# Kernel tuning notes

Hardware: AMD Instinct MI355X
Metric: run time of the kernel (lower is better)

## Reference

```python
import jax, jax.numpy as jnp
import numpy as np

B, SQ, SK, D = 8, 4096, 4096, 128


def setup_inputs() -> dict:
    key = jax.random.key(0)
    kq, kk, kv = jax.random.split(key, 3)
    return {
        "q1": jax.random.normal(kq, (B, SQ, D), dtype=jnp.float32),
        "k1": jax.random.normal(kk, (B, SK, D), dtype=jnp.float32),
        "v1": jax.random.normal(kv, (B, SK, D), dtype=jnp.float32),
        "inv_scale_factor": jnp.float32(np.sqrt(D)),  # QK is divided by this
        "dropout_p": jnp.float32(0.1),
        "dropout_m": jnp.float32(0.1),
        "dropout_inplace": 1,  # no-op in functional JAX
    }


def reference(q1, k1, v1, inv_scale_factor, dropout_p, dropout_m, dropout_inplace):
    # qk = q1 @ k1^T ; scaled = qk / inv_scale_factor ; softmax over keys
    qk = jnp.einsum("bqd,bkd->bqk", q1, k1)
    softmax_qk = jax.nn.softmax(qk / inv_scale_factor, axis=-1)
    # torch: mask = F.dropout(ones_like(sm), p) -> bernoulli(1-p)/(1-p)
    keep = jax.random.bernoulli(jax.random.key(42), 1.0 - dropout_p, softmax_qk.shape)
    mask = keep.astype(softmax_qk.dtype) / (1.0 - dropout_p)
    # non-standard: divide by (1 - dropout_m) instead of (1 - dropout_p)
    dropout_qk = softmax_qk * mask / (1.0 - dropout_m)
    return jnp.einsum("bqk,bkd->bqd", dropout_qk, v1)
```

## Files before the change

kernel.cpp:

```cpp
#include <hip/hip_runtime.h>
#include <stdint.h>

#define Bn  8
#define SQn 4096
#define SKn 4096
#define Dn  128
#define QTn 64
#define KTn 64

typedef __attribute__((ext_vector_type(8))) short short8;
typedef __attribute__((ext_vector_type(4))) short short4v;
typedef __attribute__((ext_vector_type(4))) float f32x4;

__device__ __forceinline__ short f2bf(float f) {
  uint32_t x = __float_as_uint(f);
  uint32_t r = (x + 0x7FFFu + ((x >> 16) & 1u)) >> 16;
  return (short)r;
}

__device__ __forceinline__ uint32_t rotl32(uint32_t x, int r) {
  return __builtin_amdgcn_alignbit(x, x, (32 - r) & 31);
}

__device__ __forceinline__ uint32_t tf2x32_xor(uint32_t x0, uint32_t x1) {
  const uint32_t k0 = 0u, k1 = 42u, k2 = 0x1BD11BF0u;
  x0 += k0; x1 += k1;
#define TFR(r) { x0 += x1; x1 = rotl32(x1, r); x1 ^= x0; }
  TFR(13) TFR(15) TFR(26) TFR(6)  x0 += k1; x1 += k2 + 1u;
  TFR(17) TFR(29) TFR(16) TFR(24) x0 += k2; x1 += k0 + 2u;
  TFR(13) TFR(15) TFR(26) TFR(6)  x0 += k0; x1 += k1 + 3u;
  TFR(17) TFR(29) TFR(16) TFR(24) x0 += k1; x1 += k2 + 4u;
  TFR(13) TFR(15) TFR(26) TFR(6)  x0 += k2; x1 += k0 + 5u;
#undef TFR
  return x0 ^ x1;
}

template <int N>
__device__ __forceinline__ float ror16(float x) {
  int xi = __float_as_int(x);
  int r = __builtin_amdgcn_update_dpp(xi, xi, 0x120 | N, 0xF, 0xF, false);
  return __int_as_float(r);
}
__device__ __forceinline__ float redmax16(float x) {
  x = fmaxf(x, ror16<8>(x)); x = fmaxf(x, ror16<4>(x));
  x = fmaxf(x, ror16<2>(x)); x = fmaxf(x, ror16<1>(x));
  return x;
}
__device__ __forceinline__ float redsum16(float x) {
  x += ror16<8>(x); x += ror16<4>(x); x += ror16<2>(x); x += ror16<1>(x);
  return x;
}

__global__ __launch_bounds__(256, 2) void attn(
    const float* __restrict__ Qg, const float* __restrict__ Kg, const float* __restrict__ Vg,
    const float* __restrict__ p_inv, const float* __restrict__ p_pd, const float* __restrict__ p_pm,
    float* __restrict__ Out) {
  __shared__ __align__(16) short Kt[KTn * Dn];
  __shared__ __align__(16) short Vt[Dn * KTn];
  __shared__ __align__(16) short Pt[QTn * 72];

  const int tid = threadIdx.x;
  const int w = tid >> 6;
  const int lane = tid & 63;
  const int m = lane & 15;
  const int h = lane >> 4;
  const int gid = blockIdx.x;
  const int b = gid & 7;
  const int q0 = (gid >> 3) * QTn;

  const float rscale = 1.0f / p_inv[0];
  const float pd = p_pd[0], pm = p_pm[0];
  const uint32_t ithr = (uint32_t)ceilf((1.0f - pd) * 8388608.0f);
  const float oscale_c = 1.0f / ((1.0f - pd) * (1.0f - pm));

  short8 qf[4];
  {
    const float* qp = Qg + ((size_t)(b * SQn + q0 + w * 16 + m)) * Dn;
#pragma unroll
    for (int c = 0; c < 4; c++) {
      float4 a = *reinterpret_cast<const float4*>(qp + c * 32 + h * 8);
      float4 a2 = *reinterpret_cast<const float4*>(qp + c * 32 + h * 8 + 4);
      short8 v;
      v[0] = f2bf(a.x * rscale);  v[1] = f2bf(a.y * rscale);
      v[2] = f2bf(a.z * rscale);  v[3] = f2bf(a.w * rscale);
      v[4] = f2bf(a2.x * rscale); v[5] = f2bf(a2.y * rscale);
      v[6] = f2bf(a2.z * rscale); v[7] = f2bf(a2.w * rscale);
      qf[c] = v;
    }
  }

  f32x4 acc[8];
#pragma unroll
  for (int dt = 0; dt < 8; dt++) acc[dt] = (f32x4){0.f, 0.f, 0.f, 0.f};
  float m_run[4], l_run[4];
  uint32_t rowb[4];
#pragma unroll
  for (int r = 0; r < 4; r++) {
    m_run[r] = -1e30f;
    l_run[r] = 0.f;
    rowb[r] = (uint32_t)(b * SQn + q0 + w * 16 + 4 * h + r) * (uint32_t)SKn;
  }

  const size_t kvbase = (size_t)b * SKn * Dn;

  float4 kreg[8], vreg[8];
  auto issue_loads = [&](int kt) {
    const float* kp = Kg + kvbase + (size_t)kt * KTn * Dn;
    const float* vp = Vg + kvbase + (size_t)kt * KTn * Dn;
#pragma unroll
    for (int p = 0; p < 8; p++) {
      int idx = p * 256 + tid;
      kreg[p] = *reinterpret_cast<const float4*>(kp + (idx >> 5) * Dn + (idx & 31) * 4);
    }
#pragma unroll
    for (int p = 0; p < 4; p++) {
      int idx = p * 256 + tid;
      int kp2 = idx >> 5, dq = idx & 31;
      vreg[2 * p]     = *reinterpret_cast<const float4*>(vp + (2 * kp2) * Dn + dq * 4);
      vreg[2 * p + 1] = *reinterpret_cast<const float4*>(vp + (2 * kp2 + 1) * Dn + dq * 4);
    }
  };
  auto write_tiles = [&]() {
#pragma unroll
    for (int p = 0; p < 8; p++) {
      int idx = p * 256 + tid;
      int row = idx >> 5, dq = idx & 31;
      float4 x = kreg[p];
      short4v sv;
      sv[0] = f2bf(x.x); sv[1] = f2bf(x.y); sv[2] = f2bf(x.z); sv[3] = f2bf(x.w);
      *reinterpret_cast<short4v*>(&Kt[row * 128 + ((dq * 4) ^ ((row & 7) << 3))]) = sv;
    }
#pragma unroll
    for (int p = 0; p < 4; p++) {
      int idx = p * 256 + tid;
      int kp2 = idx >> 5, dq = idx & 31;
      int swz = (dq & 7) << 3;
      float4 v0 = vreg[2 * p], v1 = vreg[2 * p + 1];
      const float* f0 = &v0.x;
      const float* f1 = &v1.x;
#pragma unroll
      for (int i = 0; i < 4; i++) {
        int d = dq * 4 + i;
        uint32_t pk = ((uint32_t)(uint16_t)f2bf(f0[i])) |
                      (((uint32_t)(uint16_t)f2bf(f1[i])) << 16);
        *reinterpret_cast<uint32_t*>(&Vt[d * 64 + ((2 * kp2) ^ swz)]) = pk;
      }
    }
  };

  issue_loads(0);

  for (int kt = 0; kt < SKn / KTn; kt++) {
    __syncthreads();
    write_tiles();
    if (kt + 1 < SKn / KTn) issue_loads(kt + 1);
    __syncthreads();

    f32x4 sfr[4];
#pragma unroll
    for (int t = 0; t < 4; t++) {
      f32x4 s = (f32x4){0.f, 0.f, 0.f, 0.f};
      int krow = t * 16 + m;
      int swzk = (krow & 7) << 3;
#pragma unroll
      for (int c = 0; c < 4; c++) {
        short8 kf = *reinterpret_cast<const short8*>(
            &Kt[krow * 128 + ((c * 32 + h * 8) ^ swzk)]);
        s = __builtin_amdgcn_mfma_f32_16x16x32_bf16(qf[c], kf, s, 0, 0, 0);
      }
      sfr[t] = s;
    }

    float oscl[4];
    float pv[4][4];
#pragma unroll
    for (int r = 0; r < 4; r++) {
      float s0 = sfr[0][r], s1 = sfr[1][r], s2 = sfr[2][r], s3 = sfr[3][r];
      float tmax = redmax16(fmaxf(fmaxf(s0, s1), fmaxf(s2, s3)));
      float mnew = fmaxf(m_run[r], tmax);
      float al = __expf(m_run[r] - mnew);
      float e0 = __expf(s0 - mnew), e1 = __expf(s1 - mnew);
      float e2 = __expf(s2 - mnew), e3 = __expf(s3 - mnew);
      float ts = redsum16(e0 + e1 + e2 + e3);
      l_run[r] = l_run[r] * al + ts;
      m_run[r] = mnew;
      oscl[r] = al;
      pv[0][r] = e0; pv[1][r] = e1; pv[2][r] = e2; pv[3][r] = e3;
    }
#pragma unroll
    for (int dt = 0; dt < 8; dt++) {
#pragma unroll
      for (int r = 0; r < 4; r++) acc[dt][r] *= oscl[r];
    }

    const uint32_t kbase = (uint32_t)(kt * 64 + m);
#pragma unroll
    for (int r = 0; r < 4; r++) {
      int qrow = w * 16 + 4 * h + r;
      int psw = (qrow & 8) << 1;
      uint32_t nb = rowb[r] + kbase;
#pragma unroll
      for (int t = 0; t < 4; t++) {
        uint32_t bits = tf2x32_xor(0u, nb + (uint32_t)(t * 16));
        bool kp = (bits >> 9) < ithr;
        float pmv = kp ? pv[t][r] : 0.0f;
        Pt[qrow * 72 + ((t * 16 + m) ^ psw)] = f2bf(pmv);
      }
    }

    {
      int qr = w * 16 + m;
      int psw = (qr & 8) << 1;
#pragma unroll
      for (int c = 0; c < 2; c++) {
        short8 pa = *reinterpret_cast<const short8*>(&Pt[qr * 72 + ((c * 32 + h * 8) ^ psw)]);
#pragma unroll
        for (int dt = 0; dt < 8; dt++) {
          int d = dt * 16 + m;
          short8 vb = *reinterpret_cast<const short8*>(
              &Vt[d * 64 + ((c * 32 + h * 8) ^ (((d >> 2) & 7) << 3))]);
          acc[dt] = __builtin_amdgcn_mfma_f32_16x16x32_bf16(pa, vb, acc[dt], 0, 0, 0);
        }
      }
    }
  }

#pragma unroll
  for (int r = 0; r < 4; r++) {
    float os = oscale_c / l_run[r];
    float* op = Out + (size_t)(b * SQn + q0 + w * 16 + 4 * h + r) * Dn;
#pragma unroll
    for (int dt = 0; dt < 8; dt++) op[dt * 16 + m] = acc[dt][r] * os;
  }
}

extern "C" void kernel_launch(void* const* d_in, const int* in_sizes, int n_in,
                              void* d_out, int out_size, void* d_ws, size_t ws_size,
                              hipStream_t stream) {
  const float* Qg = (const float*)d_in[0];
  const float* Kg = (const float*)d_in[1];
  const float* Vg = (const float*)d_in[2];
  const float* p_inv = (const float*)d_in[3];
  const float* p_pd = (const float*)d_in[4];
  const float* p_pm = (const float*)d_in[5];
  float* Out = (float*)d_out;

  attn<<<dim3(512), dim3(256), 0, stream>>>(Qg, Kg, Vg, p_inv, p_pd, p_pm, Out);
}
```

Baseline: 496.3 us.

## Pre-convert K/V to swizzled bf16 workspace and stream tiles via direct LDS loads

Adds a prep kernel that converts K and V to bf16 once, pre-swizzles them and transposes V, writing the results to the workspace. The attention kernel then double-buffers 16 KB tiles with global_load_lds straight into shared memory. This removes the per-block redundant fp32 loads, the conversions and the register staging, and drops one barrier per iteration. In exchange it adds an extra kernel launch, a write and re-read of the workspace, and doubles LDS use, which may limit occupancy. The original kernel is kept as a fallback for when the workspace is too small.

```diff
diff --git a/kernel.cpp b/kernel.cpp
--- a/kernel.cpp
+++ b/kernel.cpp
@@ -7,6 +7,7 @@
 #define Dn  128
 #define QTn 64
 #define KTn 64
+static constexpr size_t KV_BYTES = 8ull * 4096 * 128 * 2;
 
 typedef __attribute__((ext_vector_type(8))) short short8;
 typedef __attribute__((ext_vector_type(4))) short short4v;
@@ -51,12 +52,67 @@
   return x;
 }
 
+__device__ __forceinline__ void gload16(const void* g, void* l) {
+  __builtin_amdgcn_global_load_lds(
+      (const __attribute__((address_space(1))) uint32_t*)g,
+      (__attribute__((address_space(3))) uint32_t*)l, 16, 0, 0);
+}
+
+__global__ __launch_bounds__(256) void prep(const float* __restrict__ K,
+                                            const float* __restrict__ V,
+                                            short* __restrict__ Kws,
+                                            short* __restrict__ Vws) {
+  const int blk = blockIdx.x;
+  const int t = blk & 511;
+  const int tid = threadIdx.x;
+  if (blk < 512) {
+    const float* src = K + (size_t)t * (KTn * Dn);
+    short* dst = Kws + (size_t)t * (KTn * Dn);
+#pragma unroll
+    for (int i = 0; i < 4; i++) {
+      int idx = i * 2048 + tid * 8;
+      int row = idx >> 7, colp = idx & 127;
+      int colsrc = colp ^ ((row & 7) << 3);
+      float4 a  = *reinterpret_cast<const float4*>(src + row * Dn + colsrc);
+      float4 a2 = *reinterpret_cast<const float4*>(src + row * Dn + colsrc + 4);
+      short8 v;
+      v[0] = f2bf(a.x);  v[1] = f2bf(a.y);  v[2] = f2bf(a.z);  v[3] = f2bf(a.w);
+      v[4] = f2bf(a2.x); v[5] = f2bf(a2.y); v[6] = f2bf(a2.z); v[7] = f2bf(a2.w);
+      *reinterpret_cast<short8*>(dst + idx) = v;
+    }
+  } else {
+    __shared__ short Vl[KTn][Dn + 2];
+    const float* src = V + (size_t)t * (KTn * Dn);
+#pragma unroll
+    for (int i = 0; i < 8; i++) {
+      int idx = i * 1024 + tid * 4;
+      int k = idx >> 7, d = idx & 127;
+      float4 a = *reinterpret_cast<const float4*>(src + idx);
+      Vl[k][d + 0] = f2bf(a.x); Vl[k][d + 1] = f2bf(a.y);
+      Vl[k][d + 2] = f2bf(a.z); Vl[k][d + 3] = f2bf(a.w);
+    }
+    __syncthreads();
+    short* dst = Vws + (size_t)t * (KTn * Dn);
+#pragma unroll
+    for (int i = 0; i < 4; i++) {
+      int o = i * 2048 + tid * 8;
+      int d = o >> 6, kp = o & 63;
+      int ksrc = kp ^ (((d >> 2) & 7) << 3);
+      short8 v;
+#pragma unroll
+      for (int j = 0; j < 8; j++) v[j] = Vl[ksrc + j][d];
+      *reinterpret_cast<short8*>(dst + o) = v;
+    }
+  }
+}
+
 __global__ __launch_bounds__(256, 2) void attn(
-    const float* __restrict__ Qg, const float* __restrict__ Kg, const float* __restrict__ Vg,
-    const float* __restrict__ p_inv, const float* __restrict__ p_pd, const float* __restrict__ p_pm,
-    float* __restrict__ Out) {
-  __shared__ __align__(16) short Kt[KTn * Dn];
-  __shared__ __align__(16) short Vt[Dn * KTn];
+    const float* __restrict__ Qg, const short* __restrict__ Kws,
+    const short* __restrict__ Vws,
+    const float* __restrict__ p_inv, const float* __restrict__ p_pd,
+    const float* __restrict__ p_pm, float* __restrict__ Out) {
+  __shared__ __align__(16) short Kt[2][KTn * Dn];
+  __shared__ __align__(16) short Vt[2][Dn * KTn];
   __shared__ __align__(16) short Pt[QTn * 72];
 
   const int tid = threadIdx.x;
@@ -101,60 +157,26 @@
     rowb[r] = (uint32_t)(b * SQn + q0 + w * 16 + 4 * h + r) * (uint32_t)SKn;
   }
 
-  const size_t kvbase = (size_t)b * SKn * Dn;
-
-  float4 kreg[8], vreg[8];
-  auto issue_loads = [&](int kt) {
-    const float* kp = Kg + kvbase + (size_t)kt * KTn * Dn;
-    const float* vp = Vg + kvbase + (size_t)kt * KTn * Dn;
-#pragma unroll
-    for (int p = 0; p < 8; p++) {
-      int idx = p * 256 + tid;
-      kreg[p] = *reinterpret_cast<const float4*>(kp + (idx >> 5) * Dn + (idx & 31) * 4);
-    }
-#pragma unroll
-    for (int p = 0; p < 4; p++) {
-      int idx = p * 256 + tid;
-      int kp2 = idx >> 5, dq = idx & 31;
-      vreg[2 * p]     = *reinterpret_cast<const float4*>(vp + (2 * kp2) * Dn + dq * 4);
-      vreg[2 * p + 1] = *reinterpret_cast<const float4*>(vp + (2 * kp2 + 1) * Dn + dq * 4);
+  const char* Kbase = (const char*)(Kws + (size_t)(b * 64) * (KTn * Dn));
+  const char* Vbase = (const char*)(Vws + (size_t)(b * 64) * (KTn * Dn));
+
+  auto stage = [&](int kt, int buf) {
+    const char* ks = Kbase + (size_t)kt * 16384;
+    const char* vs = Vbase + (size_t)kt * 16384;
+#pragma unroll
+    for (int i = 0; i < 4; i++) {
+      int off = w * 4096 + i * 1024;
+      gload16(ks + off + lane * 16, (char*)&Kt[buf][0] + off);
+      gload16(vs + off + lane * 16, (char*)&Vt[buf][0] + off);
     }
   };
-  auto write_tiles = [&]() {
-#pragma unroll
-    for (int p = 0; p < 8; p++) {
-      int idx = p * 256 + tid;
-      int row = idx >> 5, dq = idx & 31;
-      float4 x = kreg[p];
-      short4v sv;
-      sv[0] = f2bf(x.x); sv[1] = f2bf(x.y); sv[2] = f2bf(x.z); sv[3] = f2bf(x.w);
-      *reinterpret_cast<short4v*>(&Kt[row * 128 + ((dq * 4) ^ ((row & 7) << 3))]) = sv;
-    }
-#pragma unroll
-    for (int p = 0; p < 4; p++) {
-      int idx = p * 256 + tid;
-      int kp2 = idx >> 5, dq = idx & 31;
-      int swz = (dq & 7) << 3;
-      float4 v0 = vreg[2 * p], v1 = vreg[2 * p + 1];
-      const float* f0 = &v0.x;
-      const float* f1 = &v1.x;
-#pragma unroll
-      for (int i = 0; i < 4; i++) {
-        int d = dq * 4 + i;
-        uint32_t pk = ((uint32_t)(uint16_t)f2bf(f0[i])) |
-                      (((uint32_t)(uint16_t)f2bf(f1[i])) << 16);
-        *reinterpret_cast<uint32_t*>(&Vt[d * 64 + ((2 * kp2) ^ swz)]) = pk;
-      }
-    }
-  };
-
-  issue_loads(0);
+
+  stage(0, 0);
 
   for (int kt = 0; kt < SKn / KTn; kt++) {
+    const int cur = kt & 1;
     __syncthreads();
-    write_tiles();
-    if (kt + 1 < SKn / KTn) issue_loads(kt + 1);
-    __syncthreads();
+    if (kt + 1 < SKn / KTn) stage(kt + 1, cur ^ 1);
 
     f32x4 sfr[4];
 #pragma unroll
@@ -165,7 +187,7 @@
 #pragma unroll
       for (int c = 0; c < 4; c++) {
         short8 kf = *reinterpret_cast<const short8*>(
-            &Kt[krow * 128 + ((c * 32 + h * 8) ^ swzk)]);
+            &Kt[cur][krow * 128 + ((c * 32 + h * 8) ^ swzk)]);
         s = __builtin_amdgcn_mfma_f32_16x16x32_bf16(qf[c], kf, s, 0, 0, 0);
       }
       sfr[t] = s;
@@ -218,13 +240,182 @@
         for (int dt = 0; dt < 8; dt++) {
           int d = dt * 16 + m;
           short8 vb = *reinterpret_cast<const short8*>(
+              &Vt[cur][d * 64 + ((c * 32 + h * 8) ^ (((d >> 2) & 7) << 3))]);
+          acc[dt] = __builtin_amdgcn_mfma_f32_16x16x32_bf16(pa, vb, acc[dt], 0, 0, 0);
+        }
+      }
+    }
+  }
+
+#pragma unroll
+  for (int r = 0; r < 4; r++) {
+    float os = oscale_c / l_run[r];
+    float* op = Out + (size_t)(b * SQn + q0 + w * 16 + 4 * h + r) * Dn;
+#pragma unroll
+    for (int dt = 0; dt < 8; dt++) op[dt * 16 + m] = acc[dt][r] * os;
+  }
+}
+
+__global__ __launch_bounds__(256, 2) void attn_fb(
+    const float* __restrict__ Qg, const float* __restrict__ Kg, const float* __restrict__ Vg,
+    const float* __restrict__ p_inv, const float* __restrict__ p_pd, const float* __restrict__ p_pm,
+    float* __restrict__ Out) {
+  __shared__ __align__(16) short Kt[KTn * Dn];
+  __shared__ __align__(16) short Vt[Dn * KTn];
+  __shared__ __align__(16) short Pt[QTn * 72];
+  const int tid = threadIdx.x;
+  const int w = tid >> 6;
+  const int lane = tid & 63;
+  const int m = lane & 15;
+  const int h = lane >> 4;
+  const int gid = blockIdx.x;
+  const int b = gid & 7;
+  const int q0 = (gid >> 3) * QTn;
+  const float rscale = 1.0f / p_inv[0];
+  const float pd = p_pd[0], pm = p_pm[0];
+  const uint32_t ithr = (uint32_t)ceilf((1.0f - pd) * 8388608.0f);
+  const float oscale_c = 1.0f / ((1.0f - pd) * (1.0f - pm));
+  short8 qf[4];
+  {
+    const float* qp = Qg + ((size_t)(b * SQn + q0 + w * 16 + m)) * Dn;
+#pragma unroll
+    for (int c = 0; c < 4; c++) {
+      float4 a = *reinterpret_cast<const float4*>(qp + c * 32 + h * 8);
+      float4 a2 = *reinterpret_cast<const float4*>(qp + c * 32 + h * 8 + 4);
+      short8 v;
+      v[0] = f2bf(a.x * rscale);  v[1] = f2bf(a.y * rscale);
+      v[2] = f2bf(a.z * rscale);  v[3] = f2bf(a.w * rscale);
+      v[4] = f2bf(a2.x * rscale); v[5] = f2bf(a2.y * rscale);
+      v[6] = f2bf(a2.z * rscale); v[7] = f2bf(a2.w * rscale);
+      qf[c] = v;
+    }
+  }
+  f32x4 acc[8];
+#pragma unroll
+  for (int dt = 0; dt < 8; dt++) acc[dt] = (f32x4){0.f, 0.f, 0.f, 0.f};
+  float m_run[4], l_run[4];
+  uint32_t rowb[4];
+#pragma unroll
+  for (int r = 0; r < 4; r++) {
+    m_run[r] = -1e30f; l_run[r] = 0.f;
+    rowb[r] = (uint32_t)(b * SQn + q0 + w * 16 + 4 * h + r) * (uint32_t)SKn;
+  }
+  const size_t kvbase = (size_t)b * SKn * Dn;
+  float4 kreg[8], vreg[8];
+  auto issue_loads = [&](int kt) {
+    const float* kp = Kg + kvbase + (size_t)kt * KTn * Dn;
+    const float* vp = Vg + kvbase + (size_t)kt * KTn * Dn;
+#pragma unroll
+    for (int p = 0; p < 8; p++) {
+      int idx = p * 256 + tid;
+      kreg[p] = *reinterpret_cast<const float4*>(kp + (idx >> 5) * Dn + (idx & 31) * 4);
+    }
+#pragma unroll
+    for (int p = 0; p < 4; p++) {
+      int idx = p * 256 + tid;
+      int kp2 = idx >> 5, dq = idx & 31;
+      vreg[2 * p]     = *reinterpret_cast<const float4*>(vp + (2 * kp2) * Dn + dq * 4);
+      vreg[2 * p + 1] = *reinterpret_cast<const float4*>(vp + (2 * kp2 + 1) * Dn + dq * 4);
+    }
+  };
+  auto write_tiles = [&]() {
+#pragma unroll
+    for (int p = 0; p < 8; p++) {
+      int idx = p * 256 + tid;
+      int row = idx >> 5, dq = idx & 31;
+      float4 x = kreg[p];
+      short4v sv;
+      sv[0] = f2bf(x.x); sv[1] = f2bf(x.y); sv[2] = f2bf(x.z); sv[3] = f2bf(x.w);
+      *reinterpret_cast<short4v*>(&Kt[row * 128 + ((dq * 4) ^ ((row & 7) << 3))]) = sv;
+    }
+#pragma unroll
+    for (int p = 0; p < 4; p++) {
+      int idx = p * 256 + tid;
+      int kp2 = idx >> 5, dq = idx & 31;
+      int swz = (dq & 7) << 3;
+      float4 v0 = vreg[2 * p], v1 = vreg[2 * p + 1];
+      const float* f0 = &v0.x;
+      const float* f1 = &v1.x;
+#pragma unroll
+      for (int i = 0; i < 4; i++) {
+        int d = dq * 4 + i;
+        uint32_t pk = ((uint32_t)(uint16_t)f2bf(f0[i])) |
+                      (((uint32_t)(uint16_t)f2bf(f1[i])) << 16);
+        *reinterpret_cast<uint32_t*>(&Vt[d * 64 + ((2 * kp2) ^ swz)]) = pk;
+      }
+    }
+  };
+  issue_loads(0);
+  for (int kt = 0; kt < SKn / KTn; kt++) {
+    __syncthreads();
+    write_tiles();
+    if (kt + 1 < SKn / KTn) issue_loads(kt + 1);
+    __syncthreads();
+    f32x4 sfr[4];
+#pragma unroll
+    for (int t = 0; t < 4; t++) {
+      f32x4 s = (f32x4){0.f, 0.f, 0.f, 0.f};
+      int krow = t * 16 + m;
+      int swzk = (krow & 7) << 3;
+#pragma unroll
+      for (int c = 0; c < 4; c++) {
+        short8 kf = *reinterpret_cast<const short8*>(
+            &Kt[krow * 128 + ((c * 32 + h * 8) ^ swzk)]);
+        s = __builtin_amdgcn_mfma_f32_16x16x32_bf16(qf[c], kf, s, 0, 0, 0);
+      }
+      sfr[t] = s;
+    }
+    float oscl[4];
+    float pv[4][4];
+#pragma unroll
+    for (int r = 0; r < 4; r++) {
+      float s0 = sfr[0][r], s1 = sfr[1][r], s2 = sfr[2][r], s3 = sfr[3][r];
+      float tmax = redmax16(fmaxf(fmaxf(s0, s1), fmaxf(s2, s3)));
+      float mnew = fmaxf(m_run[r], tmax);
+      float al = __expf(m_run[r] - mnew);
+      float e0 = __expf(s0 - mnew), e1 = __expf(s1 - mnew);
+      float e2 = __expf(s2 - mnew), e3 = __expf(s3 - mnew);
+      float ts = redsum16(e0 + e1 + e2 + e3);
+      l_run[r] = l_run[r] * al + ts;
+      m_run[r] = mnew;
+      oscl[r] = al;
+      pv[0][r] = e0; pv[1][r] = e1; pv[2][r] = e2; pv[3][r] = e3;
+    }
+#pragma unroll
+    for (int dt = 0; dt < 8; dt++) {
+#pragma unroll
+      for (int r = 0; r < 4; r++) acc[dt][r] *= oscl[r];
+    }
+    const uint32_t kbase = (uint32_t)(kt * 64 + m);
+#pragma unroll
+    for (int r = 0; r < 4; r++) {
+      int qrow = w * 16 + 4 * h + r;
+      int psw = (qrow & 8) << 1;
+      uint32_t nb = rowb[r] + kbase;
+#pragma unroll
+      for (int t = 0; t < 4; t++) {
+        uint32_t bits = tf2x32_xor(0u, nb + (uint32_t)(t * 16));
+        bool kp = (bits >> 9) < ithr;
+        float pmv = kp ? pv[t][r] : 0.0f;
+        Pt[qrow * 72 + ((t * 16 + m) ^ psw)] = f2bf(pmv);
+      }
+    }
+    {
+      int qr = w * 16 + m;
+      int psw = (qr & 8) << 1;
+#pragma unroll
+      for (int c = 0; c < 2; c++) {
+        short8 pa = *reinterpret_cast<const short8*>(&Pt[qr * 72 + ((c * 32 + h * 8) ^ psw)]);
+#pragma unroll
+        for (int dt = 0; dt < 8; dt++) {
+          int d = dt * 16 + m;
+          short8 vb = *reinterpret_cast<const short8*>(
               &Vt[d * 64 + ((c * 32 + h * 8) ^ (((d >> 2) & 7) << 3))]);
           acc[dt] = __builtin_amdgcn_mfma_f32_16x16x32_bf16(pa, vb, acc[dt], 0, 0, 0);
         }
       }
     }
   }
-
 #pragma unroll
   for (int r = 0; r < 4; r++) {
     float os = oscale_c / l_run[r];
@@ -245,5 +436,12 @@
   const float* p_pm = (const float*)d_in[5];
   float* Out = (float*)d_out;
 
-  attn<<<dim3(512), dim3(256), 0, stream>>>(Qg, Kg, Vg, p_inv, p_pd, p_pm, Out);
-}
+  if (ws_size >= 2 * KV_BYTES) {
+    short* Kws = (short*)d_ws;
+    short* Vws = (short*)((char*)d_ws + KV_BYTES);
+    prep<<<dim3(1024), dim3(256), 0, stream>>>(Kg, Vg, Kws, Vws);
+    attn<<<dim3(512), dim3(256), 0, stream>>>(Qg, Kws, Vws, p_inv, p_pd, p_pm, Out);
+  } else {
+    attn_fb<<<dim3(512), dim3(256), 0, stream>>>(Qg, Kg, Vg, p_inv, p_pd, p_pm, Out);
+  }
+}
```

After: 465.8 us. -6.1%, faster.
